# Optimization experiments

Hardware: AMD Instinct MI355X
Metric: run time of the kernel (lower is better)

The kernel has to match this reference:

```python
import jax, jax.numpy as jnp
import numpy as np
import math

B, T, C = 2, 2048, 2048
H, KV, HD = 16, 4, 128  # num_heads, num_kv_heads, head_dim
REP = H // KV


def _rope_tables(T, hd, base=10000.0):
    inv_freq = 1.0 / (base ** (np.arange(0, hd, 2, dtype=np.float32) / hd))  # [hd/2]
    t = np.arange(T, dtype=np.float32)
    freqs = np.outer(t, inv_freq)                 # [T, hd/2]
    emb = np.concatenate([freqs, freqs], axis=-1)  # [T, hd]
    return jnp.asarray(np.cos(emb)), jnp.asarray(np.sin(emb))


def setup_inputs() -> dict:
    key = jax.random.key(0)
    ks = jax.random.split(key, 5)
    cos, sin = _rope_tables(T, HD)
    std = 0.02
    return {
        "x": jax.random.normal(ks[0], (B, T, C), dtype=jnp.float32),
        "cos": cos,
        "sin": sin,
        "Wq": jax.random.normal(ks[1], (C, H * HD), dtype=jnp.float32) * std,
        "Wk": jax.random.normal(ks[2], (C, KV * HD), dtype=jnp.float32) * std,
        "Wv": jax.random.normal(ks[3], (C, KV * HD), dtype=jnp.float32) * std,
        "Wo": jax.random.normal(ks[4], (H * HD, C), dtype=jnp.float32) * std,
    }


def _rotate_half(t):
    h = t.shape[-1] // 2
    return jnp.concatenate([-t[..., h:], t[..., :h]], axis=-1)


def reference(x, cos, sin, Wq, Wk, Wv, Wo):
    Bx, Tx, Cx = x.shape
    q = (x @ Wq).reshape(Bx, Tx, H, HD).transpose(0, 2, 1, 3)   # [B,H,T,hd]
    k = (x @ Wk).reshape(Bx, Tx, KV, HD).transpose(0, 2, 1, 3)  # [B,KV,T,hd]
    v = (x @ Wv).reshape(Bx, Tx, KV, HD).transpose(0, 2, 1, 3)
    c = cos[None, None]  # [1,1,T,hd]
    s = sin[None, None]
    q = q * c + _rotate_half(q) * s
    k = k * c + _rotate_half(k) * s
    # repeat_kv: expand KV heads to H heads (interleave within groups)
    k = jnp.repeat(k, REP, axis=1)  # [B,H,T,hd]
    v = jnp.repeat(v, REP, axis=1)
    scores = jnp.einsum("bhqd,bhkd->bhqk", q, k) / math.sqrt(HD)
    causal = jnp.triu(jnp.full((Tx, Tx), float("-inf"), dtype=scores.dtype), k=1)
    scores = jax.nn.softmax(scores + causal[None, None], axis=-1)
    out = jnp.einsum("bhqk,bhkd->bhqd", scores, v)  # [B,H,T,hd]
    out = out.transpose(0, 2, 1, 3).reshape(Bx, Tx, H * HD)
    return out @ Wo
```

## Files before the change

### kernel.cpp

```cpp
#include <hip/hip_runtime.h>
#include <hip/hip_bf16.h>
#include <math.h>

typedef __bf16 bf16_t;
typedef __bf16 bf16x8 __attribute__((ext_vector_type(8)));
typedef float f32x4 __attribute__((ext_vector_type(4)));

constexpr int Bc = 2, Tc = 2048, Cdim = 2048, Hc = 16, KVc = 4, HDc = 128;
constexpr int Mc = Bc * Tc;
constexpr int Nqkv = 3072;

typedef const __attribute__((address_space(1))) void* as1_cptr;
typedef __attribute__((address_space(3))) void* as3_ptr;

__device__ __forceinline__ void gload_lds16(const bf16_t* g, bf16_t* l) {
  __builtin_amdgcn_global_load_lds((as1_cptr)(const void*)g, (as3_ptr)(void*)l, 16, 0, 0);
}

__device__ __forceinline__ unsigned int cvt_pk_bf16(float lo, float hi) {
  unsigned int r;
  asm("v_cvt_pk_bf16_f32 %0, %1, %2" : "=v"(r) : "v"(lo), "v"(hi));
  return r;
}
__device__ __forceinline__ void perm32swap(unsigned int& a, unsigned int& b) {
  asm("v_permlane32_swap_b32 %0, %1" : "+v"(a), "+v"(b));
}
__device__ __forceinline__ void perm16swap(unsigned int& a, unsigned int& b) {
  asm("v_permlane16_swap_b32 %0, %1" : "+v"(a), "+v"(b));
}

__global__ void k_cvt_bf16(const float* __restrict__ in, bf16_t* __restrict__ out) {
  int i = (blockIdx.x * 256 + threadIdx.x) * 8;
  float4 a = *(const float4*)(in + i);
  float4 b = *(const float4*)(in + i + 4);
  bf16x8 v;
  v[0] = (bf16_t)a.x; v[1] = (bf16_t)a.y; v[2] = (bf16_t)a.z; v[3] = (bf16_t)a.w;
  v[4] = (bf16_t)b.x; v[5] = (bf16_t)b.y; v[6] = (bf16_t)b.z; v[7] = (bf16_t)b.w;
  *(bf16x8*)(out + i) = v;
}

__global__ void k_w_trans(const float* __restrict__ W, bf16_t* __restrict__ Wt,
                          int K, int N) {
  __shared__ alignas(16) bf16_t tile[64][72];
  const int k0 = blockIdx.x * 64, n0 = blockIdx.y * 64;
  const int t = threadIdx.x;
#pragma unroll
  for (int i = 0; i < 4; ++i) {
    int idx = t + i * 256;
    int r = idx >> 4;
    int c4 = (idx & 15) * 4;
    float4 v = *(const float4*)(W + (size_t)(k0 + r) * N + n0 + c4);
    tile[r][c4 + 0] = (bf16_t)v.x; tile[r][c4 + 1] = (bf16_t)v.y;
    tile[r][c4 + 2] = (bf16_t)v.z; tile[r][c4 + 3] = (bf16_t)v.w;
  }
  __syncthreads();
#pragma unroll
  for (int i = 0; i < 4; ++i) {
    int idx = t + i * 256;
    int n = idx >> 4;
    int kc = (idx & 15) * 4;
    alignas(8) bf16_t o[4];
#pragma unroll
    for (int j = 0; j < 4; ++j) o[j] = tile[kc + j][n];
    *(uint2*)(Wt + (size_t)(n0 + n) * K + k0 + kc) = *(uint2*)o;
  }
}

template <typename OutT>
__global__ __launch_bounds__(256, 2) void k_gemm_bt(
    const bf16_t* __restrict__ A, const bf16_t* __restrict__ Bt,
    OutT* __restrict__ Cout, int M, int N, int K) {
  __shared__ alignas(16) bf16_t Ash[128 * 64];
  __shared__ alignas(16) bf16_t Bsh[128 * 64];
  const int tid = threadIdx.x;
  const int wave = tid >> 6, lane = tid & 63;
  const int col = lane & 15, quad = lane >> 4;
  const int m0 = blockIdx.y * 128, n0 = blockIdx.x * 128;
  const int wr = wave >> 1, wc = wave & 1;

  f32x4 acc[4][4];
#pragma unroll
  for (int i = 0; i < 4; ++i)
#pragma unroll
    for (int j = 0; j < 4; ++j) acc[i][j] = f32x4{0.f, 0.f, 0.f, 0.f};

  const int lrow = lane >> 3;
  const int lkc8 = (lane & 7) ^ lrow;

  for (int k0 = 0; k0 < K; k0 += 64) {
    __syncthreads();
#pragma unroll
    for (int i = 0; i < 4; ++i) {
      const int rb = wave * 32 + i * 8;
      gload_lds16(A + (size_t)(m0 + rb + lrow) * K + k0 + lkc8 * 8, Ash + rb * 64);
      gload_lds16(Bt + (size_t)(n0 + rb + lrow) * K + k0 + lkc8 * 8, Bsh + rb * 64);
    }
    __syncthreads();
#pragma unroll
    for (int kc = 0; kc < 2; ++kc) {
      bf16x8 af[4], bfr[4];
#pragma unroll
      for (int mt = 0; mt < 4; ++mt) {
        const int m = wr * 64 + mt * 16 + col;
        const int slot = (kc * 4 + quad) ^ (m & 7);
        af[mt] = *(const bf16x8*)(Ash + m * 64 + slot * 8);
      }
#pragma unroll
      for (int nt = 0; nt < 4; ++nt) {
        const int n = wc * 64 + nt * 16 + col;
        const int slot = (kc * 4 + quad) ^ (n & 7);
        bfr[nt] = *(const bf16x8*)(Bsh + n * 64 + slot * 8);
      }
#pragma unroll
      for (int mt = 0; mt < 4; ++mt)
#pragma unroll
        for (int nt = 0; nt < 4; ++nt)
          acc[mt][nt] = __builtin_amdgcn_mfma_f32_16x16x32_bf16(
              af[mt], bfr[nt], acc[mt][nt], 0, 0, 0);
    }
  }
#pragma unroll
  for (int mt = 0; mt < 4; ++mt)
#pragma unroll
    for (int i = 0; i < 4; ++i) {
      const int row = m0 + wr * 64 + mt * 16 + quad * 4 + i;
#pragma unroll
      for (int nt = 0; nt < 4; ++nt)
        Cout[(size_t)row * N + n0 + wc * 64 + nt * 16 + col] = (OutT)acc[mt][nt][i];
    }
}

__global__ void k_rope2(const bf16_t* __restrict__ in, const float* __restrict__ cs,
                        const float* __restrict__ sn, bf16_t* __restrict__ outQ,
                        bf16_t* __restrict__ outK) {
  const int idx = blockIdx.x * 256 + threadIdx.x;
  const int d = idx & 63;
  const int hh = (idx >> 6) % 20;
  const int bt = idx / (64 * 20);
  const int t = bt & (Tc - 1);
  const int b = bt >> 11;
  const bool isQ = hh < 16;
  const int h = isQ ? hh : hh - 16;
  const int colb = isQ ? h * HDc : 2048 + h * HDc;
  const size_t bi = (size_t)(b * Tc + t) * Nqkv + colb;
  const float x0 = (float)in[bi + d];
  const float x1 = (float)in[bi + d + 64];
  const float c0 = cs[t * HDc + d], c1 = cs[t * HDc + d + 64];
  const float s0 = sn[t * HDc + d], s1 = sn[t * HDc + d + 64];
  bf16_t* op = isQ ? outQ + ((size_t)(b * Hc + h) * Tc + t) * HDc
                   : outK + ((size_t)(b * KVc + h) * Tc + t) * HDc;
  op[d]      = (bf16_t)(x0 * c0 - x1 * s0);
  op[d + 64] = (bf16_t)(x1 * c1 + x0 * s1);
}

__global__ void k_vtrans(const bf16_t* __restrict__ v, bf16_t* __restrict__ vt,
                         int in_stride, int col_off) {
  __shared__ alignas(16) bf16_t tile[64][136];
  const int t0 = blockIdx.x * 64;
  const int kv = blockIdx.y, b = blockIdx.z;
  const int tid = threadIdx.x;
#pragma unroll
  for (int i = 0; i < 4; ++i) {
    int idx = tid + i * 256;
    int r = idx >> 4;
    int ch = idx & 15;
    const bf16_t* gp = v + (size_t)(b * Tc + t0 + r) * in_stride + col_off + kv * HDc + ch * 8;
    *(uint4*)&tile[r][ch * 8] = *(const uint4*)gp;
  }
  __syncthreads();
#pragma unroll
  for (int i = 0; i < 4; ++i) {
    int idx = tid + i * 256;
    int d = idx >> 3;
    int tc = idx & 7;
    alignas(16) bf16_t o[8];
#pragma unroll
    for (int j = 0; j < 8; ++j) o[j] = tile[tc * 8 + j][d];
    bf16_t* gp = vt + ((size_t)(b * KVc + kv) * HDc + d) * Tc + t0 + tc * 8;
    *(uint4*)gp = *(uint4*)o;
  }
}

__global__ __launch_bounds__(256, 2) void k_attn(
    const bf16_t* __restrict__ Qp, const bf16_t* __restrict__ Kp,
    const bf16_t* __restrict__ Vt, bf16_t* __restrict__ Oout) {
  constexpr float sc2 = 0.08838834764831845f * 1.4426950408889634f;
  __shared__ alignas(16) bf16_t Ksh[2][64 * 128];
  __shared__ alignas(16) bf16_t Vsh[2][128 * 64];

  const int i2 = blockIdx.x, h = blockIdx.y, b = blockIdx.z;
  const int kvh = h >> 2;
  const int tid = threadIdx.x, wave = tid >> 6, lane = tid & 63;
  const int col = lane & 15, quad = lane >> 4;

  const bf16_t* Kb = Kp + (size_t)(b * KVc + kvh) * Tc * HDc;
  const bf16_t* Vb = Vt + (size_t)(b * KVc + kvh) * HDc * Tc;
  const bf16_t* Qbh = Qp + (size_t)(b * Hc + h) * Tc * HDc;

  const int st_kr = lane >> 4, st_kc8 = lane & 15;
  const int st_vr = lane >> 3, st_vc8 = lane & 7;

  const int qb0 = 31 - i2, qb1 = i2;
  const int n0it = qb0 + 1;
  const int ntot = qb0 + qb1 + 2;

  int q0 = qb0 * 64 + wave * 16;
  const int qr = wave * 16 + col;

  bf16x8 qf[4];
  {
    const bf16_t* qbase = Qbh + (size_t)(q0 + col) * HDc;
#pragma unroll
    for (int kc = 0; kc < 4; ++kc) {
      bf16x8 raw = *(const bf16x8*)(qbase + kc * 32 + quad * 8);
#pragma unroll
      for (int e = 0; e < 8; ++e) qf[kc][e] = (bf16_t)((float)raw[e] * sc2);
    }
  }

  f32x4 o_acc[8];
#pragma unroll
  for (int nb = 0; nb < 8; ++nb) o_acc[nb] = f32x4{0.f, 0.f, 0.f, 0.f};
  float l_i = 0.f;

#pragma unroll
  for (int i = 0; i < 4; ++i) {
    const int rb = wave * 16 + i * 4;
    const int r = rb + st_kr;
    const int kc8 = st_kc8 ^ (r & 7);
    gload_lds16(Kb + (size_t)r * HDc + kc8 * 8, &Ksh[0][rb * 128]);
    const int db = wave * 32 + i * 8;
    const int d = db + st_vr;
    const int tc8 = st_vc8 ^ (d & 7);
    gload_lds16(Vb + (size_t)d * Tc + tc8 * 8, &Vsh[0][db * 64]);
  }

#pragma unroll 1
  for (int j = 0; j < ntot; ++j) {
    const int cur = j & 1;
    const bool diag = (j == qb0) || (j == ntot - 1);
    asm volatile("s_barrier" ::: "memory");
    {
      const int jn = (j + 1 < ntot) ? (j + 1) : (ntot - 1);
      const int tn = (jn < n0it) ? jn : (jn - n0it);
      const int kbn = tn * 64;
#pragma unroll
      for (int i = 0; i < 4; ++i) {
        const int rb = wave * 16 + i * 4;
        const int r = rb + st_kr;
        const int kc8 = st_kc8 ^ (r & 7);
        gload_lds16(Kb + (size_t)(kbn + r) * HDc + kc8 * 8, &Ksh[cur ^ 1][rb * 128]);
        const int db = wave * 32 + i * 8;
        const int d = db + st_vr;
        const int tc8 = st_vc8 ^ (d & 7);
        gload_lds16(Vb + (size_t)d * Tc + kbn + tc8 * 8, &Vsh[cur ^ 1][db * 64]);
      }
    }
    asm volatile("s_waitcnt vmcnt(8)" ::: "memory");
    asm volatile("s_barrier" ::: "memory");

    const bf16_t* Kc = &Ksh[cur][0];
    const bf16_t* Vc = &Vsh[cur][0];

    f32x4 st[4];
#pragma unroll
    for (int tb = 0; tb < 4; ++tb) st[tb] = f32x4{0.f, 0.f, 0.f, 0.f};
#pragma unroll
    for (int kc = 0; kc < 4; ++kc)
#pragma unroll
      for (int tb = 0; tb < 4; ++tb) {
        const int r = tb * 16 + col;
        const int slot = (kc * 4 + quad) ^ (r & 7);
        bf16x8 kf = *(const bf16x8*)(Kc + r * 128 + slot * 8);
        st[tb] = __builtin_amdgcn_mfma_f32_16x16x32_bf16(kf, qf[kc], st[tb], 0, 0, 0);
      }

    unsigned int pwrd[4][2];
#pragma unroll
    for (int tb = 0; tb < 4; ++tb) {
      const int kvb = tb * 16 + quad * 4;
      float e0 = exp2f(st[tb][0]), e1 = exp2f(st[tb][1]);
      float e2 = exp2f(st[tb][2]), e3 = exp2f(st[tb][3]);
      if (diag) {
        e0 = (kvb + 0 > qr) ? 0.f : e0;
        e1 = (kvb + 1 > qr) ? 0.f : e1;
        e2 = (kvb + 2 > qr) ? 0.f : e2;
        e3 = (kvb + 3 > qr) ? 0.f : e3;
      }
      l_i += (e0 + e1) + (e2 + e3);
      pwrd[tb][0] = cvt_pk_bf16(e0, e1);
      pwrd[tb][1] = cvt_pk_bf16(e2, e3);
    }

#pragma unroll
    for (int kc = 0; kc < 2; ++kc) {
      unsigned int a0 = pwrd[2 * kc][0], b0 = pwrd[2 * kc + 1][0];
      unsigned int a1 = pwrd[2 * kc][1], b1 = pwrd[2 * kc + 1][1];
      perm32swap(a0, b0);
      perm32swap(a1, b1);
      perm16swap(a0, b0);
      perm16swap(a1, b1);
      union { unsigned int w[4]; bf16x8 v; } u;
      u.w[0] = a0; u.w[1] = a1; u.w[2] = b0; u.w[3] = b1;
      const bf16x8 pf = u.v;
#pragma unroll
      for (int nb = 0; nb < 8; ++nb) {
        const int d = nb * 16 + col;
        const int vslot = (kc * 4 + quad) ^ (d & 7);
        bf16x8 vf = *(const bf16x8*)(Vc + d * 64 + vslot * 8);
        o_acc[nb] = __builtin_amdgcn_mfma_f32_16x16x32_bf16(pf, vf, o_acc[nb], 0, 0, 0);
      }
    }

    if (j == qb0) {
      float rs = l_i;
      rs += __shfl_xor(rs, 16);
      rs += __shfl_xor(rs, 32);
      const float inv = 1.0f / rs;
#pragma unroll
      for (int i = 0; i < 4; ++i) {
        const float iq = __shfl(inv, quad * 4 + i);
        const int qrow = q0 + quad * 4 + i;
        bf16_t* op = Oout + ((size_t)(b * Tc) + qrow) * (Hc * HDc) + h * HDc;
#pragma unroll
        for (int nb = 0; nb < 8; ++nb) op[nb * 16 + col] = (bf16_t)(o_acc[nb][i] * iq);
      }
      l_i = 0.f;
#pragma unroll
      for (int nb = 0; nb < 8; ++nb) o_acc[nb] = f32x4{0.f, 0.f, 0.f, 0.f};
      q0 = qb1 * 64 + wave * 16;
      const bf16_t* qbase = Qbh + (size_t)(q0 + col) * HDc;
#pragma unroll
      for (int kc = 0; kc < 4; ++kc) {
        bf16x8 raw = *(const bf16x8*)(qbase + kc * 32 + quad * 8);
#pragma unroll
        for (int e = 0; e < 8; ++e) qf[kc][e] = (bf16_t)((float)raw[e] * sc2);
      }
    }
  }

  {
    float rs = l_i;
    rs += __shfl_xor(rs, 16);
    rs += __shfl_xor(rs, 32);
    const float inv = 1.0f / rs;
#pragma unroll
    for (int i = 0; i < 4; ++i) {
      const float iq = __shfl(inv, quad * 4 + i);
      const int qrow = q0 + quad * 4 + i;
      bf16_t* op = Oout + ((size_t)(b * Tc) + qrow) * (Hc * HDc) + h * HDc;
#pragma unroll
      for (int nb = 0; nb < 8; ++nb) op[nb * 16 + col] = (bf16_t)(o_acc[nb][i] * iq);
    }
  }
}

extern "C" void kernel_launch(void* const* d_in, const int* in_sizes, int n_in,
                              void* d_out, int out_size, void* d_ws, size_t ws_size,
                              hipStream_t stream) {
  (void)in_sizes; (void)n_in; (void)out_size; (void)ws_size;
  const float* x    = (const float*)d_in[0];
  const float* cosT = (const float*)d_in[1];
  const float* sinT = (const float*)d_in[2];
  const float* Wq   = (const float*)d_in[3];
  const float* Wk   = (const float*)d_in[4];
  const float* Wv   = (const float*)d_in[5];
  const float* Wo   = (const float*)d_in[6];
  float* out = (float*)d_out;

  char* ws = (char*)d_ws;
  size_t off = 0;
  auto take = [&](size_t bytes) { char* p = ws + off; off += (bytes + 255) & ~(size_t)255; return p; };

  bf16_t* xb    = (bf16_t*)take((size_t)Mc * Cdim * 2);
  bf16_t* Wqkvt = (bf16_t*)take((size_t)Nqkv * Cdim * 2);
  bf16_t* Wot   = (bf16_t*)take((size_t)Cdim * (Hc * HDc) * 2);
  bf16_t* qkv   = (bf16_t*)take((size_t)Mc * Nqkv * 2);
  bf16_t* Kp    = (bf16_t*)take((size_t)Mc * (KVc * HDc) * 2);
  bf16_t* Vt    = (bf16_t*)take((size_t)Mc * (KVc * HDc) * 2);
  bf16_t* Wqt = Wqkvt;
  bf16_t* Wkt = Wqkvt + (size_t)2048 * Cdim;
  bf16_t* Wvt = Wqkvt + (size_t)2560 * Cdim;
  bf16_t* Qp   = xb;
  bf16_t* attn = qkv;

  k_cvt_bf16<<<dim3((Mc * Cdim) / 2048), dim3(256), 0, stream>>>(x, xb);
  k_w_trans<<<dim3(Cdim / 64, 2048 / 64), dim3(256), 0, stream>>>(Wq, Wqt, Cdim, 2048);
  k_w_trans<<<dim3(Cdim / 64, 512 / 64), dim3(256), 0, stream>>>(Wk, Wkt, Cdim, 512);
  k_w_trans<<<dim3(Cdim / 64, 512 / 64), dim3(256), 0, stream>>>(Wv, Wvt, Cdim, 512);
  k_w_trans<<<dim3((Hc * HDc) / 64, Cdim / 64), dim3(256), 0, stream>>>(Wo, Wot, Hc * HDc, Cdim);
  k_gemm_bt<bf16_t><<<dim3(Nqkv / 128, Mc / 128), dim3(256), 0, stream>>>(
      xb, Wqkvt, qkv, Mc, Nqkv, Cdim);
  k_rope2<<<dim3((Bc * Tc * 20 * 64) / 256), dim3(256), 0, stream>>>(
      qkv, cosT, sinT, Qp, Kp);
  k_vtrans<<<dim3(Tc / 64, KVc, Bc), dim3(256), 0, stream>>>(qkv, Vt, Nqkv, 2560);
  k_attn<<<dim3(16, Hc, Bc), dim3(256), 0, stream>>>(Qp, Kp, Vt, attn);
  k_gemm_bt<float><<<dim3(Cdim / 128, Mc / 128), dim3(256), 0, stream>>>(
      attn, Wot, out, Mc, Cdim, Hc * HDc);
}
```

Baseline: 306.7 us.

## Replace GEMM with 256x256 tile, 8-wave double-buffered pipelined kernel

Swaps the 128x128 single-buffered bf16 GEMM for a 256x256-tile kernel using 512 threads. It double-buffers A/B tiles in LDS with direct global-to-LDS loads, interleaves the staging of the next K-step with MFMA phases, and orders them with explicit vmcnt waits and barriers. It also raises wave priority around the MFMA blocks and remaps workgroup IDs in an XCD-aware way for cache locality. This aims to hide global load latency and raise arithmetic intensity, at the cost of 128KB of LDS, many more accumulator registers, and fewer workgroups (192 and 128), which may underfill the 256 CUs.

```diff
diff --git a/kernel.cpp b/kernel.cpp
--- a/kernel.cpp
+++ b/kernel.cpp
@@ -67,63 +67,129 @@
 }
 
 template <typename OutT>
-__global__ __launch_bounds__(256, 2) void k_gemm_bt(
+__global__ __launch_bounds__(512, 2) void k_gemm256(
     const bf16_t* __restrict__ A, const bf16_t* __restrict__ Bt,
     OutT* __restrict__ Cout, int M, int N, int K) {
-  __shared__ alignas(16) bf16_t Ash[128 * 64];
-  __shared__ alignas(16) bf16_t Bsh[128 * 64];
+  __shared__ alignas(16) bf16_t Ash[2][2][128 * 64];
+  __shared__ alignas(16) bf16_t Bsh[2][2][128 * 64];
   const int tid = threadIdx.x;
   const int wave = tid >> 6, lane = tid & 63;
   const int col = lane & 15, quad = lane >> 4;
-  const int m0 = blockIdx.y * 128, n0 = blockIdx.x * 128;
-  const int wr = wave >> 1, wc = wave & 1;
-
-  f32x4 acc[4][4];
-#pragma unroll
-  for (int i = 0; i < 4; ++i)
+  const int wr = wave >> 2, wc = wave & 3;
+
+  const int nwg = gridDim.x * gridDim.y;
+  int wg = blockIdx.y * gridDim.x + blockIdx.x;
+  wg = (wg & 7) * (nwg >> 3) + (wg >> 3);
+  const int bx = wg % gridDim.x, by = wg / gridDim.x;
+  const int m0 = by * 256, n0 = bx * 256;
+
+  const int stg_row = wave * 8 + (lane >> 3);
+  const int stg_sl8 = ((lane & 7) ^ (lane >> 3)) * 8;
+
+  auto stageA = [&](int tb, int r, int sidx) {
+#pragma unroll
+    for (int h = 0; h < 2; ++h)
+      gload_lds16(A + (size_t)(m0 + h * 128 + r * 64 + stg_row) * K + sidx * 64 + stg_sl8,
+                  &Ash[tb][h][(r * 64 + wave * 8) * 64]);
+  };
+  auto stageB = [&](int tb, int h, int sidx) {
+#pragma unroll
+    for (int r = 0; r < 2; ++r)
+      gload_lds16(Bt + (size_t)(n0 + h * 128 + r * 64 + stg_row) * K + sidx * 64 + stg_sl8,
+                  &Bsh[tb][h][(r * 64 + wave * 8) * 64]);
+  };
+  auto frag = [&](const bf16_t* H, int r, int kc) {
+    return *(const bf16x8*)(H + r * 64 + (((kc * 4 + quad) ^ (r & 7)) * 8));
+  };
+
+  f32x4 acc[8][4];
+#pragma unroll
+  for (int i = 0; i < 8; ++i)
 #pragma unroll
     for (int j = 0; j < 4; ++j) acc[i][j] = f32x4{0.f, 0.f, 0.f, 0.f};
 
-  const int lrow = lane >> 3;
-  const int lkc8 = (lane & 7) ^ lrow;
-
-  for (int k0 = 0; k0 < K; k0 += 64) {
-    __syncthreads();
+  const int NSTEP = K >> 6;
+
+  stageB(0, 0, 0); stageB(0, 1, 0);
+  stageA(0, 0, 0); stageA(0, 1, 0);
+  stageB(1, 0, 1); stageB(1, 1, 1);
+  asm volatile("s_waitcnt vmcnt(6)" ::: "memory");
+  asm volatile("s_barrier" ::: "memory");
+
+#pragma unroll 1
+  for (int s = 0; s < NSTEP; ++s) {
+    const int buf = s & 1;
+    const bf16_t* AH = &Ash[buf][wr][0];
+    const bf16_t* BH = &Bsh[buf][wc >> 1][0];
+    const int nrow = (wc & 1) * 64;
+    bf16x8 bfr[2][4], af[4];
+
+#pragma unroll
+    for (int mt = 0; mt < 4; ++mt) af[mt] = frag(AH, mt * 16 + col, 0);
+#pragma unroll
+    for (int nt = 0; nt < 4; ++nt) bfr[0][nt] = frag(BH, nrow + nt * 16 + col, 0);
+    if (s + 1 < NSTEP) stageA(buf ^ 1, 0, s + 1);
+    asm volatile("s_barrier" ::: "memory");
+    __builtin_amdgcn_s_setprio(1);
+#pragma unroll
+    for (int mt = 0; mt < 4; ++mt)
+#pragma unroll
+      for (int nt = 0; nt < 4; ++nt)
+        acc[mt][nt] = __builtin_amdgcn_mfma_f32_16x16x32_bf16(af[mt], bfr[0][nt], acc[mt][nt], 0, 0, 0);
+    __builtin_amdgcn_s_setprio(0);
+    asm volatile("s_barrier" ::: "memory");
+
+#pragma unroll
+    for (int mt = 0; mt < 4; ++mt) af[mt] = frag(AH, mt * 16 + col, 1);
+#pragma unroll
+    for (int nt = 0; nt < 4; ++nt) bfr[1][nt] = frag(BH, nrow + nt * 16 + col, 1);
+    if (s + 1 < NSTEP) stageA(buf ^ 1, 1, s + 1);
+    asm volatile("s_barrier" ::: "memory");
+    __builtin_amdgcn_s_setprio(1);
+#pragma unroll
+    for (int mt = 0; mt < 4; ++mt)
+#pragma unroll
+      for (int nt = 0; nt < 4; ++nt)
+        acc[mt][nt] = __builtin_amdgcn_mfma_f32_16x16x32_bf16(af[mt], bfr[1][nt], acc[mt][nt], 0, 0, 0);
+    __builtin_amdgcn_s_setprio(0);
+    if (s == NSTEP - 1) { asm volatile("s_waitcnt vmcnt(0)" ::: "memory"); }
+    else                { asm volatile("s_waitcnt vmcnt(8)" ::: "memory"); }
+    asm volatile("s_barrier" ::: "memory");
+
+#pragma unroll
+    for (int mt = 0; mt < 4; ++mt) af[mt] = frag(AH, (mt + 4) * 16 + col, 0);
+    if (s + 2 < NSTEP) stageB(buf, 0, s + 2);
+    asm volatile("s_barrier" ::: "memory");
+    __builtin_amdgcn_s_setprio(1);
+#pragma unroll
+    for (int mt = 0; mt < 4; ++mt)
+#pragma unroll
+      for (int nt = 0; nt < 4; ++nt)
+        acc[mt + 4][nt] = __builtin_amdgcn_mfma_f32_16x16x32_bf16(af[mt], bfr[0][nt], acc[mt + 4][nt], 0, 0, 0);
+    __builtin_amdgcn_s_setprio(0);
+    asm volatile("s_barrier" ::: "memory");
+
+#pragma unroll
+    for (int mt = 0; mt < 4; ++mt) af[mt] = frag(AH, (mt + 4) * 16 + col, 1);
+    if (s + 2 < NSTEP) stageB(buf, 1, s + 2);
+    asm volatile("s_barrier" ::: "memory");
+    __builtin_amdgcn_s_setprio(1);
+#pragma unroll
+    for (int mt = 0; mt < 4; ++mt)
+#pragma unroll
+      for (int nt = 0; nt < 4; ++nt)
+        acc[mt + 4][nt] = __builtin_amdgcn_mfma_f32_16x16x32_bf16(af[mt], bfr[1][nt], acc[mt + 4][nt], 0, 0, 0);
+    __builtin_amdgcn_s_setprio(0);
+    if (s == NSTEP - 2)      { asm volatile("s_waitcnt vmcnt(2)" ::: "memory"); }
+    else if (s < NSTEP - 2)  { asm volatile("s_waitcnt vmcnt(6)" ::: "memory"); }
+    asm volatile("s_barrier" ::: "memory");
+  }
+
+#pragma unroll
+  for (int mt = 0; mt < 8; ++mt)
 #pragma unroll
     for (int i = 0; i < 4; ++i) {
-      const int rb = wave * 32 + i * 8;
-      gload_lds16(A + (size_t)(m0 + rb + lrow) * K + k0 + lkc8 * 8, Ash + rb * 64);
-      gload_lds16(Bt + (size_t)(n0 + rb + lrow) * K + k0 + lkc8 * 8, Bsh + rb * 64);
-    }
-    __syncthreads();
-#pragma unroll
-    for (int kc = 0; kc < 2; ++kc) {
-      bf16x8 af[4], bfr[4];
-#pragma unroll
-      for (int mt = 0; mt < 4; ++mt) {
-        const int m = wr * 64 + mt * 16 + col;
-        const int slot = (kc * 4 + quad) ^ (m & 7);
-        af[mt] = *(const bf16x8*)(Ash + m * 64 + slot * 8);
-      }
-#pragma unroll
-      for (int nt = 0; nt < 4; ++nt) {
-        const int n = wc * 64 + nt * 16 + col;
-        const int slot = (kc * 4 + quad) ^ (n & 7);
-        bfr[nt] = *(const bf16x8*)(Bsh + n * 64 + slot * 8);
-      }
-#pragma unroll
-      for (int mt = 0; mt < 4; ++mt)
-#pragma unroll
-        for (int nt = 0; nt < 4; ++nt)
-          acc[mt][nt] = __builtin_amdgcn_mfma_f32_16x16x32_bf16(
-              af[mt], bfr[nt], acc[mt][nt], 0, 0, 0);
-    }
-  }
-#pragma unroll
-  for (int mt = 0; mt < 4; ++mt)
-#pragma unroll
-    for (int i = 0; i < 4; ++i) {
-      const int row = m0 + wr * 64 + mt * 16 + quad * 4 + i;
+      const int row = m0 + wr * 128 + mt * 16 + quad * 4 + i;
 #pragma unroll
       for (int nt = 0; nt < 4; ++nt)
         Cout[(size_t)row * N + n0 + wc * 64 + nt * 16 + col] = (OutT)acc[mt][nt][i];
@@ -389,12 +455,12 @@
   k_w_trans<<<dim3(Cdim / 64, 512 / 64), dim3(256), 0, stream>>>(Wk, Wkt, Cdim, 512);
   k_w_trans<<<dim3(Cdim / 64, 512 / 64), dim3(256), 0, stream>>>(Wv, Wvt, Cdim, 512);
   k_w_trans<<<dim3((Hc * HDc) / 64, Cdim / 64), dim3(256), 0, stream>>>(Wo, Wot, Hc * HDc, Cdim);
-  k_gemm_bt<bf16_t><<<dim3(Nqkv / 128, Mc / 128), dim3(256), 0, stream>>>(
+  k_gemm256<bf16_t><<<dim3(Nqkv / 256, Mc / 256), dim3(512), 0, stream>>>(
       xb, Wqkvt, qkv, Mc, Nqkv, Cdim);
   k_rope2<<<dim3((Bc * Tc * 20 * 64) / 256), dim3(256), 0, stream>>>(
       qkv, cosT, sinT, Qp, Kp);
   k_vtrans<<<dim3(Tc / 64, KVc, Bc), dim3(256), 0, stream>>>(qkv, Vt, Nqkv, 2560);
   k_attn<<<dim3(16, Hc, Bc), dim3(256), 0, stream>>>(Qp, Kp, Vt, attn);
-  k_gemm_bt<float><<<dim3(Cdim / 128, Mc / 128), dim3(256), 0, stream>>>(
+  k_gemm256<float><<<dim3(Cdim / 256, Mc / 256), dim3(512), 0, stream>>>(
       attn, Wot, out, Mc, Cdim, Hc * HDc);
 }
```

Result: slower. 324.9 us (+5.9%).

## Fuse RoPE and V transpose into QKV GEMM epilogue, merge prep kernels

Applied to the files above, without the earlier changes.

Merges the x conversion and four weight-transpose launches into one prep kernel with block-range dispatch. Adds a dedicated QKV GEMM whose per-wave tile (32x128) holds a whole head's columns, so RoPE is applied in the epilogue and Q/K are written directly in head-major layout. V is written transposed straight from the accumulators. This removes the intermediate qkv buffer round trip and two extra kernels, at the cost of a different wave tiling (2x8 MFMA tiles), scattered epilogue stores and a less coalesced V transpose write.

```diff
diff --git a/kernel.cpp b/kernel.cpp
--- a/kernel.cpp
+++ b/kernel.cpp
@@ -29,20 +29,29 @@
   asm("v_permlane16_swap_b32 %0, %1" : "+v"(a), "+v"(b));
 }
 
-__global__ void k_cvt_bf16(const float* __restrict__ in, bf16_t* __restrict__ out) {
-  int i = (blockIdx.x * 256 + threadIdx.x) * 8;
-  float4 a = *(const float4*)(in + i);
-  float4 b = *(const float4*)(in + i + 4);
-  bf16x8 v;
-  v[0] = (bf16_t)a.x; v[1] = (bf16_t)a.y; v[2] = (bf16_t)a.z; v[3] = (bf16_t)a.w;
-  v[4] = (bf16_t)b.x; v[5] = (bf16_t)b.y; v[6] = (bf16_t)b.z; v[7] = (bf16_t)b.w;
-  *(bf16x8*)(out + i) = v;
-}
-
-__global__ void k_w_trans(const float* __restrict__ W, bf16_t* __restrict__ Wt,
-                          int K, int N) {
+__global__ void k_prep(const float* __restrict__ x, bf16_t* __restrict__ xb,
+                       const float* __restrict__ Wq, const float* __restrict__ Wk,
+                       const float* __restrict__ Wv, const float* __restrict__ Wo,
+                       bf16_t* __restrict__ Wqt, bf16_t* __restrict__ Wkt,
+                       bf16_t* __restrict__ Wvt, bf16_t* __restrict__ Wot) {
   __shared__ alignas(16) bf16_t tile[64][72];
-  const int k0 = blockIdx.x * 64, n0 = blockIdx.y * 64;
+  int bid = blockIdx.x;
+  if (bid < 4096) {
+    int i = (bid * 256 + threadIdx.x) * 8;
+    float4 a = *(const float4*)(x + i);
+    float4 b = *(const float4*)(x + i + 4);
+    bf16x8 v;
+    v[0] = (bf16_t)a.x; v[1] = (bf16_t)a.y; v[2] = (bf16_t)a.z; v[3] = (bf16_t)a.w;
+    v[4] = (bf16_t)b.x; v[5] = (bf16_t)b.y; v[6] = (bf16_t)b.z; v[7] = (bf16_t)b.w;
+    *(bf16x8*)(xb + i) = v;
+    return;
+  }
+  bid -= 4096;
+  const float* W; bf16_t* Wt; int K, N, k0, n0;
+  if (bid < 1024)      { W = Wq; Wt = Wqt; K = 2048; N = 2048; k0 = (bid >> 5) * 64; n0 = (bid & 31) * 64; }
+  else if (bid < 1280) { bid -= 1024; W = Wk; Wt = Wkt; K = 2048; N = 512; k0 = (bid >> 3) * 64; n0 = (bid & 7) * 64; }
+  else if (bid < 1536) { bid -= 1280; W = Wv; Wt = Wvt; K = 2048; N = 512; k0 = (bid >> 3) * 64; n0 = (bid & 7) * 64; }
+  else                 { bid -= 1536; W = Wo; Wt = Wot; K = 2048; N = 2048; k0 = (bid >> 5) * 64; n0 = (bid & 31) * 64; }
   const int t = threadIdx.x;
 #pragma unroll
   for (int i = 0; i < 4; ++i) {
@@ -66,10 +75,9 @@
   }
 }
 
-template <typename OutT>
 __global__ __launch_bounds__(256, 2) void k_gemm_bt(
     const bf16_t* __restrict__ A, const bf16_t* __restrict__ Bt,
-    OutT* __restrict__ Cout, int M, int N, int K) {
+    float* __restrict__ Cout, int M, int N, int K) {
   __shared__ alignas(16) bf16_t Ash[128 * 64];
   __shared__ alignas(16) bf16_t Bsh[128 * 64];
   const int tid = threadIdx.x;
@@ -126,58 +134,101 @@
       const int row = m0 + wr * 64 + mt * 16 + quad * 4 + i;
 #pragma unroll
       for (int nt = 0; nt < 4; ++nt)
-        Cout[(size_t)row * N + n0 + wc * 64 + nt * 16 + col] = (OutT)acc[mt][nt][i];
-    }
-}
-
-__global__ void k_rope2(const bf16_t* __restrict__ in, const float* __restrict__ cs,
-                        const float* __restrict__ sn, bf16_t* __restrict__ outQ,
-                        bf16_t* __restrict__ outK) {
-  const int idx = blockIdx.x * 256 + threadIdx.x;
-  const int d = idx & 63;
-  const int hh = (idx >> 6) % 20;
-  const int bt = idx / (64 * 20);
-  const int t = bt & (Tc - 1);
-  const int b = bt >> 11;
-  const bool isQ = hh < 16;
-  const int h = isQ ? hh : hh - 16;
-  const int colb = isQ ? h * HDc : 2048 + h * HDc;
-  const size_t bi = (size_t)(b * Tc + t) * Nqkv + colb;
-  const float x0 = (float)in[bi + d];
-  const float x1 = (float)in[bi + d + 64];
-  const float c0 = cs[t * HDc + d], c1 = cs[t * HDc + d + 64];
-  const float s0 = sn[t * HDc + d], s1 = sn[t * HDc + d + 64];
-  bf16_t* op = isQ ? outQ + ((size_t)(b * Hc + h) * Tc + t) * HDc
-                   : outK + ((size_t)(b * KVc + h) * Tc + t) * HDc;
-  op[d]      = (bf16_t)(x0 * c0 - x1 * s0);
-  op[d + 64] = (bf16_t)(x1 * c1 + x0 * s1);
-}
-
-__global__ void k_vtrans(const bf16_t* __restrict__ v, bf16_t* __restrict__ vt,
-                         int in_stride, int col_off) {
-  __shared__ alignas(16) bf16_t tile[64][136];
-  const int t0 = blockIdx.x * 64;
-  const int kv = blockIdx.y, b = blockIdx.z;
+        Cout[(size_t)row * N + n0 + wc * 64 + nt * 16 + col] = acc[mt][nt][i];
+    }
+}
+
+__global__ __launch_bounds__(256, 2) void k_gemm_qkv(
+    const bf16_t* __restrict__ A, const bf16_t* __restrict__ Bt,
+    const float* __restrict__ cs, const float* __restrict__ sn,
+    bf16_t* __restrict__ Qp, bf16_t* __restrict__ Kp, bf16_t* __restrict__ Vt) {
+  constexpr int K = Cdim;
+  __shared__ alignas(16) bf16_t Ash[128 * 64];
+  __shared__ alignas(16) bf16_t Bsh[128 * 64];
   const int tid = threadIdx.x;
-#pragma unroll
-  for (int i = 0; i < 4; ++i) {
-    int idx = tid + i * 256;
-    int r = idx >> 4;
-    int ch = idx & 15;
-    const bf16_t* gp = v + (size_t)(b * Tc + t0 + r) * in_stride + col_off + kv * HDc + ch * 8;
-    *(uint4*)&tile[r][ch * 8] = *(const uint4*)gp;
-  }
-  __syncthreads();
-#pragma unroll
-  for (int i = 0; i < 4; ++i) {
-    int idx = tid + i * 256;
-    int d = idx >> 3;
-    int tc = idx & 7;
-    alignas(16) bf16_t o[8];
-#pragma unroll
-    for (int j = 0; j < 8; ++j) o[j] = tile[tc * 8 + j][d];
-    bf16_t* gp = vt + ((size_t)(b * KVc + kv) * HDc + d) * Tc + t0 + tc * 8;
-    *(uint4*)gp = *(uint4*)o;
+  const int wave = tid >> 6, lane = tid & 63;
+  const int col = lane & 15, quad = lane >> 4;
+  const int m0 = blockIdx.y * 128, n0 = blockIdx.x * 128;
+
+  f32x4 acc[2][8];
+#pragma unroll
+  for (int i = 0; i < 2; ++i)
+#pragma unroll
+    for (int j = 0; j < 8; ++j) acc[i][j] = f32x4{0.f, 0.f, 0.f, 0.f};
+
+  const int lrow = lane >> 3;
+  const int lkc8 = (lane & 7) ^ lrow;
+
+  for (int k0 = 0; k0 < K; k0 += 64) {
+    __syncthreads();
+#pragma unroll
+    for (int i = 0; i < 4; ++i) {
+      const int rb = wave * 32 + i * 8;
+      gload_lds16(A + (size_t)(m0 + rb + lrow) * K + k0 + lkc8 * 8, Ash + rb * 64);
+      gload_lds16(Bt + (size_t)(n0 + rb + lrow) * K + k0 + lkc8 * 8, Bsh + rb * 64);
+    }
+    __syncthreads();
+#pragma unroll
+    for (int kc = 0; kc < 2; ++kc) {
+      bf16x8 af[2], bfr[8];
+#pragma unroll
+      for (int mt = 0; mt < 2; ++mt) {
+        const int m = wave * 32 + mt * 16 + col;
+        const int slot = (kc * 4 + quad) ^ (m & 7);
+        af[mt] = *(const bf16x8*)(Ash + m * 64 + slot * 8);
+      }
+#pragma unroll
+      for (int nt = 0; nt < 8; ++nt) {
+        const int n = nt * 16 + col;
+        const int slot = (kc * 4 + quad) ^ (n & 7);
+        bfr[nt] = *(const bf16x8*)(Bsh + n * 64 + slot * 8);
+      }
+#pragma unroll
+      for (int mt = 0; mt < 2; ++mt)
+#pragma unroll
+        for (int nt = 0; nt < 8; ++nt)
+          acc[mt][nt] = __builtin_amdgcn_mfma_f32_16x16x32_bf16(
+              af[mt], bfr[nt], acc[mt][nt], 0, 0, 0);
+    }
+  }
+
+  const int bx = n0 >> 7;
+  if (bx < 20) {
+    const bool isQ = bx < 16;
+#pragma unroll
+    for (int mt = 0; mt < 2; ++mt)
+#pragma unroll
+      for (int i = 0; i < 4; ++i) {
+        const int row = m0 + wave * 32 + mt * 16 + quad * 4 + i;
+        const int b = row >> 11, t = row & (Tc - 1);
+        bf16_t* op = isQ ? Qp + ((size_t)(b * Hc + bx) * Tc + t) * HDc
+                         : Kp + ((size_t)(b * KVc + (bx - 16)) * Tc + t) * HDc;
+        const float* cr = cs + t * HDc;
+        const float* sr = sn + t * HDc;
+#pragma unroll
+        for (int nt = 0; nt < 4; ++nt) {
+          const int d = nt * 16 + col;
+          const float c = cr[d], s = sr[d];
+          const float x0 = acc[mt][nt][i], x1 = acc[mt][nt + 4][i];
+          op[d]      = (bf16_t)(x0 * c - x1 * s);
+          op[d + 64] = (bf16_t)(x1 * c + x0 * s);
+        }
+      }
+  } else {
+    const int kv = bx - 20;
+#pragma unroll
+    for (int mt = 0; mt < 2; ++mt) {
+      const int row0 = m0 + wave * 32 + mt * 16 + quad * 4;
+      const int b = row0 >> 11, t0 = row0 & (Tc - 1);
+#pragma unroll
+      for (int nt = 0; nt < 8; ++nt) {
+        const int d = nt * 16 + col;
+        alignas(8) bf16_t o[4];
+#pragma unroll
+        for (int i = 0; i < 4; ++i) o[i] = (bf16_t)acc[mt][nt][i];
+        *(uint2*)(Vt + ((size_t)(b * KVc + kv) * HDc + d) * Tc + t0) = *(uint2*)o;
+      }
+    }
   }
 }
 
@@ -375,26 +426,19 @@
   bf16_t* xb    = (bf16_t*)take((size_t)Mc * Cdim * 2);
   bf16_t* Wqkvt = (bf16_t*)take((size_t)Nqkv * Cdim * 2);
   bf16_t* Wot   = (bf16_t*)take((size_t)Cdim * (Hc * HDc) * 2);
-  bf16_t* qkv   = (bf16_t*)take((size_t)Mc * Nqkv * 2);
+  bf16_t* Qp    = (bf16_t*)take((size_t)Mc * (Hc * HDc) * 2);
   bf16_t* Kp    = (bf16_t*)take((size_t)Mc * (KVc * HDc) * 2);
   bf16_t* Vt    = (bf16_t*)take((size_t)Mc * (KVc * HDc) * 2);
   bf16_t* Wqt = Wqkvt;
   bf16_t* Wkt = Wqkvt + (size_t)2048 * Cdim;
   bf16_t* Wvt = Wqkvt + (size_t)2560 * Cdim;
-  bf16_t* Qp   = xb;
-  bf16_t* attn = qkv;
-
-  k_cvt_bf16<<<dim3((Mc * Cdim) / 2048), dim3(256), 0, stream>>>(x, xb);
-  k_w_trans<<<dim3(Cdim / 64, 2048 / 64), dim3(256), 0, stream>>>(Wq, Wqt, Cdim, 2048);
-  k_w_trans<<<dim3(Cdim / 64, 512 / 64), dim3(256), 0, stream>>>(Wk, Wkt, Cdim, 512);
-  k_w_trans<<<dim3(Cdim / 64, 512 / 64), dim3(256), 0, stream>>>(Wv, Wvt, Cdim, 512);
-  k_w_trans<<<dim3((Hc * HDc) / 64, Cdim / 64), dim3(256), 0, stream>>>(Wo, Wot, Hc * HDc, Cdim);
-  k_gemm_bt<bf16_t><<<dim3(Nqkv / 128, Mc / 128), dim3(256), 0, stream>>>(
-      xb, Wqkvt, qkv, Mc, Nqkv, Cdim);
-  k_rope2<<<dim3((Bc * Tc * 20 * 64) / 256), dim3(256), 0, stream>>>(
-      qkv, cosT, sinT, Qp, Kp);
-  k_vtrans<<<dim3(Tc / 64, KVc, Bc), dim3(256), 0, stream>>>(qkv, Vt, Nqkv, 2560);
+  bf16_t* attn = xb;
+
+  k_prep<<<dim3(4096 + 1024 + 256 + 256 + 1024), dim3(256), 0, stream>>>(
+      x, xb, Wq, Wk, Wv, Wo, Wqt, Wkt, Wvt, Wot);
+  k_gemm_qkv<<<dim3(Nqkv / 128, Mc / 128), dim3(256), 0, stream>>>(
+      xb, Wqkvt, cosT, sinT, Qp, Kp, Vt);
   k_attn<<<dim3(16, Hc, Bc), dim3(256), 0, stream>>>(Qp, Kp, Vt, attn);
-  k_gemm_bt<float><<<dim3(Cdim / 128, Mc / 128), dim3(256), 0, stream>>>(
+  k_gemm_bt<<<dim3(Cdim / 128, Mc / 128), dim3(256), 0, stream>>>(
       attn, Wot, out, Mc, Cdim, Hc * HDc);
 }
```

Result: faster. 287.4 us (-6.3%).
